# Kernel tuning notes

Measured on AMD Instinct MI355X. Metric: run time of the kernel, lower is better.

The kernel has to match this reference:

```python
import jax, jax.numpy as jnp
import numpy as np

B = 32        # num graphs
N = 512       # nodes per graph (equal-sized blocks)
HID = 512     # hidden_dim
H = 8         # num_heads
E = 262144    # num edges
ED = 16       # edge feature dim


def setup_inputs() -> dict:
    key = jax.random.key(0)
    ks = jax.random.split(key, 12)
    x = jax.random.normal(ks[0], (B * N, HID), jnp.float32)
    # contiguous, sorted graph assignment (equal-sized graphs)
    batch = jnp.repeat(jnp.arange(B, dtype=jnp.int64), N)
    # within-graph random edges
    g = jax.random.randint(ks[1], (E,), 0, B)
    src = g * N + jax.random.randint(ks[2], (E,), 0, N)
    dst = g * N + jax.random.randint(ks[3], (E,), 0, N)
    edge_index = jnp.stack([src, dst]).astype(jnp.int64)
    edge_attr = jax.random.normal(ks[4], (E, ED), jnp.float32)
    s = 1.0 / np.sqrt(HID).astype(np.float32)
    Wq = jax.random.normal(ks[5], (HID, HID), jnp.float32) * s
    Wk = jax.random.normal(ks[6], (HID, HID), jnp.float32) * s
    Wv = jax.random.normal(ks[7], (HID, HID), jnp.float32) * s
    Wo = jax.random.normal(ks[8], (HID, HID), jnp.float32) * s
    We = jax.random.normal(ks[9], (ED, H), jnp.float32) * (1.0 / np.sqrt(ED).astype(np.float32))
    bq = jnp.zeros((HID,), jnp.float32)
    bk = jnp.zeros((HID,), jnp.float32)
    bv = jnp.zeros((HID,), jnp.float32)
    bo = jnp.zeros((HID,), jnp.float32)
    be = jnp.zeros((H,), jnp.float32)
    return dict(x=x, batch=batch, edge_index=edge_index, edge_attr=edge_attr,
                Wq=Wq, bq=bq, Wk=Wk, bk=bk, Wv=Wv, bv=bv, Wo=Wo, bo=bo,
                We=We, be=be, num_graphs=B)


def reference(x, batch, edge_index, edge_attr, Wq, bq, Wk, bk, Wv, bv, Wo, bo, We, be, num_graphs):
    n_total, hid = x.shape
    n = n_total // num_graphs           # nodes per graph (equal blocks)
    hd = hid // H                       # head_dim
    scale = 1.0 / jnp.sqrt(jnp.asarray(hd, x.dtype))
    q = (x @ Wq + bq).reshape(num_graphs, n, H, hd)
    k = (x @ Wk + bk).reshape(num_graphs, n, H, hd)
    v = (x @ Wv + bv).reshape(num_graphs, n, H, hd)
    # per-graph dense scores: [B, n(query), m(key), H]
    attn = jnp.einsum('bnhd,bmhd->bnmh', q, k) * scale
    # edge-bias scatter-add (edges are intra-graph; local coords via div/mod)
    eb = edge_attr @ We + be                      # [E, H]
    b_idx = edge_index[0] // n
    loc_src = edge_index[0] % n
    loc_dst = edge_index[1] % n
    attn = attn.at[b_idx, loc_src, loc_dst].add(eb)
    # softmax over key axis (torch dim=1 of 'nmh' == axis 2 here)
    attn = jax.nn.softmax(attn, axis=2)
    out = jnp.einsum('bnmh,bmhd->bnhd', attn, v).reshape(n_total, hid)
    return out @ Wo + bo
```

## Files before the change

### kernel.cpp

```cpp
#include <hip/hip_runtime.h>
#include <stdint.h>

typedef unsigned short u16;
typedef __bf16 bf16x8 __attribute__((ext_vector_type(8)));
typedef short  short8 __attribute__((ext_vector_type(8)));
typedef float  f32x4  __attribute__((ext_vector_type(4)));
typedef float  float4v __attribute__((ext_vector_type(4)));
typedef uint32_t u32x2 __attribute__((ext_vector_type(2)));

#define NG    32
#define NPG   512
#define HIDD  512
#define NH    8
#define HD    64
#define NE    262144
#define NNODE (NG*NPG)

__device__ __forceinline__ float fexp2(float x) { return __builtin_amdgcn_exp2f(x); }

__device__ __forceinline__ u16 f2bf(float f) {
  union { float f; uint32_t u; } x; x.f = f;
  uint32_t r = x.u + 0x7FFFu + ((x.u >> 16) & 1u);
  return (u16)(r >> 16);
}
__device__ __forceinline__ float bf2f(u16 b) {
  union { uint32_t u; float f; } x; x.u = ((uint32_t)b) << 16;
  return x.f;
}
__device__ __forceinline__ uint32_t pkbf(float a, float b) {
  __bf16 x = (__bf16)a, y = (__bf16)b;
  return (uint32_t)__builtin_bit_cast(u16, x) | ((uint32_t)__builtin_bit_cast(u16, y) << 16);
}
__device__ __forceinline__ bf16x8 ldfrag(const u16* p) {
  short8 t = *(const short8*)p;
  return __builtin_bit_cast(bf16x8, t);
}
__device__ __forceinline__ f32x4 mfma16(bf16x8 a, bf16x8 b, f32x4 c) {
  return __builtin_amdgcn_mfma_f32_16x16x32_bf16(a, b, c, 0, 0, 0);
}
__device__ __forceinline__ void gl2lds16(const void* g, void* l) {
  __builtin_amdgcn_global_load_lds((const __attribute__((address_space(1))) void*)g,
                                   (__attribute__((address_space(3))) void*)l, 16, 0, 0);
}
__device__ __forceinline__ void st(u16* p, float v)   { *p = f2bf(v); }
__device__ __forceinline__ void st(float* p, float v) { *p = v; }


__global__ void k_prep(const float* __restrict__ x, u16* __restrict__ xb,
                       const float* __restrict__ W0, const float* __restrict__ W1,
                       const float* __restrict__ W2, const float* __restrict__ W3,
                       u16* __restrict__ wt,
                       const int* __restrict__ ei, int* __restrict__ counts) {
  __shared__ float tl[32][33];
  const int bid = blockIdx.x, t = threadIdx.x;
  if (bid < 4096) {
    size_t i = ((size_t)bid * 256 + t) * 8;
    float4v v0 = *(const float4v*)(x + i);
    float4v v1 = *(const float4v*)(x + i + 4);
    short8 r;
    r[0]=(short)f2bf(v0[0]); r[1]=(short)f2bf(v0[1]); r[2]=(short)f2bf(v0[2]); r[3]=(short)f2bf(v0[3]);
    r[4]=(short)f2bf(v1[0]); r[5]=(short)f2bf(v1[1]); r[6]=(short)f2bf(v1[2]); r[7]=(short)f2bf(v1[3]);
    *(short8*)(xb + i) = r;
  } else if (bid < 5120) {
    const int id2 = bid - 4096;
    const int z = id2 >> 8, rem = id2 & 255;
    const int y0 = (rem >> 4) * 32, x0 = (rem & 15) * 32;
    const float* W = z==0 ? W0 : z==1 ? W1 : z==2 ? W2 : W3;
    u16* out = wt + (size_t)z * HIDD * HIDD;
    const int tx = t & 31, ty = t >> 5;
    #pragma unroll
    for (int i = 0; i < 4; ++i) tl[ty + i*8][tx] = W[(size_t)(y0 + ty + i*8) * HIDD + x0 + tx];
    __syncthreads();
    #pragma unroll
    for (int i = 0; i < 4; ++i) out[(size_t)(x0 + ty + i*8) * HIDD + (y0 + tx)] = f2bf(tl[tx][ty + i*8]);
  } else {
    int e = (bid - 5120) * 256 + t;
    int src = ei[e];
    int dl  = ei[NE + e] & (NPG - 1);
    atomicAdd(&counts[src * 8 + (dl >> 6)], 1);
  }
}


__global__ void k_scan_u(const int* __restrict__ counts, int* __restrict__ rowstart,
                         int* __restrict__ rowend, int* __restrict__ gcur) {
  __shared__ int arr[256];
  __shared__ int basesh;
  const int t = threadIdx.x;
  const int i = blockIdx.x * 256 + t;
  const int c = counts[i];
  arr[t] = c;
  __syncthreads();
  for (int off = 1; off < 256; off <<= 1) {
    int v = (t >= off) ? arr[t - off] : 0;
    __syncthreads();
    arr[t] += v;
    __syncthreads();
  }
  const int incl = arr[t];
  if (t == 255) basesh = atomicAdd(gcur, incl);
  __syncthreads();
  const int base = basesh;
  rowstart[i] = base + incl - c;
  rowend[i]   = base + incl;
}

__global__ void k_fill(const int* __restrict__ ei, const float* __restrict__ ea,
                       const float* __restrict__ We, const float* __restrict__ be,
                       const int* __restrict__ rowstart, int* __restrict__ cursor,
                       uint32_t* __restrict__ packed) {
  __shared__ float w[128];
  __shared__ float bb[8];
  int t = threadIdx.x;
  if (t < 128) w[t] = We[t];
  if (t < 8)   bb[t] = be[t];
  __syncthreads();
  int e = blockIdx.x * 256 + t;
  int src = ei[e];
  int dl  = ei[NE + e] & (NPG - 1);
  const float* ap = ea + (size_t)e * 16;
  float a[16];
  #pragma unroll
  for (int i = 0; i < 16; i += 4) {
    float4v v = *(const float4v*)(ap + i);
    a[i]=v[0]; a[i+1]=v[1]; a[i+2]=v[2]; a[i+3]=v[3];
  }
  float acc[8];
  #pragma unroll
  for (int hh = 0; hh < 8; ++hh) acc[hh] = bb[hh];
  #pragma unroll
  for (int d = 0; d < 16; ++d)
    #pragma unroll
    for (int hh = 0; hh < 8; ++hh) acc[hh] += a[d] * w[d*8 + hh];
  int bin = src * 8 + (dl >> 6);
  int pos = atomicAdd(&cursor[bin], 1);
  size_t base = ((size_t)(rowstart[bin] + pos)) * 8;
  #pragma unroll
  for (int hh = 0; hh < 8; ++hh) {
    float m = fexp2(acc[hh] * 1.44269504089f);
    union { _Float16 hf; u16 us; } cv; cv.hf = (_Float16)m;
    packed[base + hh] = (uint32_t)(dl & 63) | ((uint32_t)cv.us << 16);
  }
}


template <typename OT, bool VOUT>
__device__ void gemm_body(u16* smem, const u16* __restrict__ A, const u16* __restrict__ Bt,
                          const float* __restrict__ bias, OT* __restrict__ C,
                          u16* __restrict__ vtg, float oscale) {
  const int tid = threadIdx.x;
  const int w = tid >> 6, l = tid & 63, lr = l & 15, lg = l >> 4;
  const int idl = blockIdx.x + (blockIdx.y << 2);
  const int nid = (idl & 7) * 64 + (idl >> 3);
  const int bn0 = (nid & 3) * 128, bm0 = (nid >> 2) * 128;
  const int wr = w >> 1, wc = w & 1;
  f32x4 acc[4][4];
  #pragma unroll
  for (int i = 0; i < 4; ++i)
    #pragma unroll
    for (int j = 0; j < 4; ++j) acc[i][j] = (f32x4){0.f, 0.f, 0.f, 0.f};

  const int o1 = w * 1024 + l * 16;
  auto stageAB = [&](int kt, int buf) {
    #pragma unroll
    for (int rnd = 0; rnd < 2; ++rnd) {
      const int o = rnd * 4096 + o1;
      const int row = o >> 6, colb = o & 63;
      gl2lds16((const char*)A  + ((size_t)(bm0 + row) * HIDD + kt * 32) * 2 + colb,
               (char*)smem + buf * 8192 + o);
      gl2lds16((const char*)Bt + ((size_t)(bn0 + row) * HIDD + kt * 32) * 2 + colb,
               (char*)smem + 16384 + buf * 8192 + o);
    }
  };

  stageAB(0, 0);
  for (int kt = 0; kt < 16; ++kt) {
    if (kt < 15) {
      stageAB(kt + 1, (kt + 1) & 1);
      asm volatile("s_waitcnt vmcnt(4)" ::: "memory");
    } else {
      asm volatile("s_waitcnt vmcnt(0)" ::: "memory");
    }
    __syncthreads();
    const u16* Ab = smem + (kt & 1) * 4096;
    const u16* Bb = smem + 8192 + (kt & 1) * 4096;
    bf16x8 af[4], bfr[4];
    #pragma unroll
    for (int i = 0; i < 4; ++i) af[i]  = ldfrag(&Ab[(wr*64 + i*16 + lr) * 32 + lg*8]);
    #pragma unroll
    for (int j = 0; j < 4; ++j) bfr[j] = ldfrag(&Bb[(wc*64 + j*16 + lr) * 32 + lg*8]);
    #pragma unroll
    for (int i = 0; i < 4; ++i)
      #pragma unroll
      for (int j = 0; j < 4; ++j)
        acc[i][j] = mfma16(af[i], bfr[j], acc[i][j]);
    __syncthreads();
  }

  if constexpr (VOUT) {
    #pragma unroll
    for (int j = 0; j < 4; ++j) {
      const int d = j * 16 + lr;
      const float bv = bias[bn0 + wc*64 + j*16 + lr];
      #pragma unroll
      for (int i = 0; i < 4; ++i) {
        const int t4 = wc * 2 + wr;
        const int byteo = t4 * 8192 + d * 128 + ((i*32 + lg*8) ^ ((d & 7) << 4));
        uint32_t lo = pkbf(acc[i][j][0] + bv, acc[i][j][1] + bv);
        uint32_t hi = pkbf(acc[i][j][2] + bv, acc[i][j][3] + bv);
        *(u32x2*)((char*)smem + byteo) = (u32x2){lo, hi};
      }
    }
    __syncthreads();
    const int b = bm0 >> 9, kt0 = (bm0 & 511) >> 6, h0 = bn0 >> 6;
    #pragma unroll
    for (int t4 = 0; t4 < 4; ++t4) {
      size_t base = ((size_t)(b * 8 + h0 + (t4 >> 1)) * 8 + kt0 + (t4 & 1)) * 4096;
      #pragma unroll
      for (int rnd = 0; rnd < 2; ++rnd) {
        int idx = rnd * 256 + tid;
        *(short8*)(vtg + base + idx * 8) = *(const short8*)&smem[t4 * 4096 + idx * 8];
      }
    }
  } else {
    #pragma unroll
    for (int j = 0; j < 4; ++j) {
      const int col = bn0 + wc*64 + j*16 + lr;
      const float bv = bias[col];
      #pragma unroll
      for (int i = 0; i < 4; ++i) {
        const int row0 = bm0 + wr*64 + i*16 + lg*4;
        #pragma unroll
        for (int q = 0; q < 4; ++q)
          st(&C[(size_t)(row0 + q) * HIDD + col], (acc[i][j][q] + bv) * oscale);
      }
    }
  }
}

__global__ __launch_bounds__(256, 3) void k_gemm_qkv(
    const u16* __restrict__ A, const u16* __restrict__ Wt,
    const float* __restrict__ b0, const float* __restrict__ b1, const float* __restrict__ b2,
    u16* __restrict__ O0, u16* __restrict__ O1, u16* __restrict__ vtg) {
  __shared__ u16 smem[16384];
  const float c1 = 0.125f * 1.44269504089f;
  int z = blockIdx.z;
  const u16* Bt = Wt + (size_t)z * HIDD * HIDD;
  if (z == 0)      gemm_body<u16, false>(smem, A, Bt, b0, O0, nullptr, c1);
  else if (z == 1) gemm_body<u16, false>(smem, A, Bt, b1, O1, nullptr, 1.0f);
  else             gemm_body<u16, true >(smem, A, Bt, b2, nullptr, vtg, 1.0f);
}

__global__ __launch_bounds__(256, 3) void k_gemm_out(
    const u16* __restrict__ A, const u16* __restrict__ Bt,
    const float* __restrict__ bias, float* __restrict__ C) {
  __shared__ u16 smem[16384];
  gemm_body<float, false>(smem, A, Bt, bias, C, nullptr, 1.0f);
}


__global__ __launch_bounds__(256, 4) void k_attn(
    const u16* __restrict__ qb, const u16* __restrict__ kb, const u16* __restrict__ vtg,
    const uint32_t* __restrict__ packed, const int* __restrict__ rowstart2,
    const int* __restrict__ rowend2, u16* __restrict__ ab) {
  __shared__ u16 kl[4096];
  __shared__ u16 vl[4096];
  __shared__ u16 pl[4][2048];
  const int tid = threadIdx.x, w = tid >> 6, l = tid & 63, lr = l & 15, lg = l >> 4;

  const int id = blockIdx.x;
  const int nid = (id & 7) * 128 + (id >> 3);
  const int q0 = (nid & 3) * 128;
  const int h  = (nid >> 2) & 7;
  const int b  = nid >> 5;
  const int bh = b * 8 + h;
  const int rbase = q0 + w * 32;
  u16* plw = &pl[w][0];
  const int pswz = (lr & 7) << 4;

  bf16x8 qf[2][2];
  #pragma unroll
  for (int g = 0; g < 2; ++g) {
    const u16* qp = qb + (size_t)(b * NPG + rbase + g * 16 + lr) * HIDD + h * HD + lg * 8;
    qf[g][0] = ldfrag(qp);
    qf[g][1] = ldfrag(qp + 32);
  }

  auto stageK = [&](int kt) {
    #pragma unroll
    for (int rnd = 0; rnd < 2; ++rnd) {
      int o = rnd * 4096 + w * 1024 + l * 16;
      int key = o >> 7, db = o & 127;
      int col = db ^ ((key & 7) << 4);
      gl2lds16((const char*)kb + ((size_t)(b * NPG + kt * 64 + key) * HIDD + h * HD) * 2 + col,
               (char*)kl + o);
    }
  };
  auto stageV = [&](int kt) {
    #pragma unroll
    for (int rnd = 0; rnd < 2; ++rnd) {
      int o = rnd * 4096 + w * 1024 + l * 16;
      gl2lds16((const char*)vtg + ((size_t)(bh * 8 + kt)) * 8192 + o,
               (char*)vl + o);
    }
  };

  float rs[2] = {0.f, 0.f};
  f32x4 oacc[2][4];
  #pragma unroll
  for (int g = 0; g < 2; ++g)
    #pragma unroll
    for (int dt = 0; dt < 4; ++dt) oacc[g][dt] = (f32x4){0.f, 0.f, 0.f, 0.f};

  stageK(0); stageV(0);

  const int ge = lg & 1, ecls = lg >> 1;
  const int egrow = b * NPG + rbase + ge * 16 + lr;
  int eA = rowstart2[egrow * 8];
  int eE = rowend2[egrow * 8];

  for (int kt = 0; kt < 8; ++kt) {
    asm volatile("s_waitcnt vmcnt(0)" ::: "memory");
    __syncthreads();

    int sN = (kt < 7) ? rowstart2[egrow * 8 + kt + 1] : 0;
    int eN = (kt < 7) ? rowend2[egrow * 8 + kt + 1] : 0;
    int s0c = (eA < eE) ? eA : 0;
    uint32_t u0 = packed[(size_t)s0c * 8 + h];

    f32x4 s4[2][4];
    __builtin_amdgcn_s_setprio(1);
    #pragma unroll
    for (int sub = 0; sub < 4; ++sub) {
      int key = sub * 16 + lr;
      bf16x8 kf0, kf1;
      {
        int db0 = ((lg * 8) * 2) ^ ((key & 7) << 4);
        int db1 = ((32 + lg * 8) * 2) ^ ((key & 7) << 4);
        kf0 = ldfrag(&kl[(key * 128 + db0) >> 1]);
        kf1 = ldfrag(&kl[(key * 128 + db1) >> 1]);
      }
      #pragma unroll
      for (int g = 0; g < 2; ++g) {
        s4[g][sub] = mfma16(kf0, qf[g][0], (f32x4){0.f, 0.f, 0.f, 0.f});
        s4[g][sub] = mfma16(kf1, qf[g][1], s4[g][sub]);
      }
    }
    __builtin_amdgcn_s_setprio(0);

    #pragma unroll
    for (int g = 0; g < 2; ++g) {
      const int prow = g * 16 + lr;
      #pragma unroll
      for (int sub = 0; sub < 4; ++sub) {
        float p0 = fexp2(s4[g][sub][0]);
        float p1 = fexp2(s4[g][sub][1]);
        float p2 = fexp2(s4[g][sub][2]);
        float p3 = fexp2(s4[g][sub][3]);
        rs[g] += (p0 + p1) + (p2 + p3);
        uint32_t lo = pkbf(p0, p1);
        uint32_t hi = pkbf(p2, p3);
        *(u32x2*)((char*)plw + prow * 128 + ((sub * 32 + lg * 8) ^ pswz)) = (u32x2){lo, hi};
      }
    }
    asm volatile("s_waitcnt lgkmcnt(0)" ::: "memory");
    __builtin_amdgcn_sched_barrier(0);

    {
      float delta = 0.f;
      const int re = ge * 16 + lr;
      uint32_t u = u0;
      for (int s = eA; s < eE; ++s) {
        uint32_t ucur = u;
        if (s + 1 < eE) u = packed[(size_t)(s + 1) * 8 + h];
        int dl = (int)(ucur & 63u);
        if ((dl & 1) == ecls) {
          union { u16 us; _Float16 hf; } cv; cv.us = (u16)(ucur >> 16);
          float mult = (float)cv.hf;
          int idx = (re * 128 + ((dl * 2) ^ pswz)) >> 1;
          float old = bf2f(plw[idx]);
          plw[idx] = f2bf(old * mult);
          delta += old * (mult - 1.0f);
        }
      }
      rs[0] += (ge == 0) ? delta : 0.f;
      rs[1] += (ge == 1) ? delta : 0.f;
    }
    asm volatile("s_waitcnt lgkmcnt(0)" ::: "memory");
    __builtin_amdgcn_sched_barrier(0);

    __builtin_amdgcn_s_setprio(1);
    #pragma unroll
    for (int ks = 0; ks < 2; ++ks) {
      bf16x8 pa0 = ldfrag(&plw[(lr * 128 + ((ks * 64 + lg * 16) ^ pswz)) >> 1]);
      bf16x8 pa1 = ldfrag(&plw[((16 + lr) * 128 + ((ks * 64 + lg * 16) ^ pswz)) >> 1]);
      #pragma unroll
      for (int dt = 0; dt < 4; ++dt) {
        int d = dt * 16 + lr;
        bf16x8 vf = ldfrag(&vl[(d * 128 + ((ks * 64 + lg * 16) ^ ((d & 7) << 4))) >> 1]);
        oacc[0][dt] = mfma16(vf, pa0, oacc[0][dt]);
        oacc[1][dt] = mfma16(vf, pa1, oacc[1][dt]);
      }
    }
    __builtin_amdgcn_s_setprio(0);

    __syncthreads();
    if (kt < 7) { stageK(kt + 1); stageV(kt + 1); }
    eA = sN; eE = eN;
  }

  #pragma unroll
  for (int g = 0; g < 2; ++g) {
    float tot = rs[g] + __shfl_xor(rs[g], 16, 64);
    tot += __shfl_xor(tot, 32, 64);
    float inv = 1.0f / tot;
    const size_t grow = (size_t)(b * NPG + rbase + g * 16 + lr);
    #pragma unroll
    for (int dt = 0; dt < 4; ++dt) {
      uint32_t lo = pkbf(oacc[g][dt][0] * inv, oacc[g][dt][1] * inv);
      uint32_t hi = pkbf(oacc[g][dt][2] * inv, oacc[g][dt][3] * inv);
      *(u32x2*)(ab + grow * HIDD + h * HD + dt * 16 + lg * 4) = (u32x2){lo, hi};
    }
  }
}


extern "C" void kernel_launch(void* const* d_in, const int* in_sizes, int n_in,
                              void* d_out, int out_size, void* d_ws, size_t ws_size,
                              hipStream_t stream) {
  const float* x  = (const float*)d_in[0];
  const int*   ei = (const int*)d_in[2];
  const float* ea = (const float*)d_in[3];
  const float* Wq = (const float*)d_in[4];  const float* bq = (const float*)d_in[5];
  const float* Wk = (const float*)d_in[6];  const float* bk = (const float*)d_in[7];
  const float* Wv = (const float*)d_in[8];  const float* bv = (const float*)d_in[9];
  const float* Wo = (const float*)d_in[10]; const float* bo = (const float*)d_in[11];
  const float* We = (const float*)d_in[12]; const float* be = (const float*)d_in[13];

  char* ws = (char*)d_ws;
  const size_t MB = 1 << 20;
  u16*  xb  = (u16*)(ws);
  u16*  wt  = (u16*)(ws + 16*MB);
  u16*  qbp = (u16*)(ws + 18*MB);
  u16*  kbp = (u16*)(ws + 34*MB);
  u16*  vtg = (u16*)(ws + 50*MB);
  uint32_t* packed = (uint32_t*)(ws + 66*MB);
  int*  rowstart2 = (int*)(ws + 74*MB);
  int*  rowend2   = (int*)(ws + 74*MB + 640*1024);
  int*  counts2  = (int*)(ws + 50*MB);
  int*  cursor2  = (int*)(ws + 50*MB + 512*1024);
  int*  gcur     = (int*)(ws + 51*MB);
  u16*  ab = xb;

  (void)hipMemsetAsync(counts2, 0, 1024 * 1024 + 64, stream);

  k_prep<<<dim3(6144), 256, 0, stream>>>(x, xb, Wq, Wk, Wv, Wo, wt, ei, counts2);
  k_scan_u<<<dim3(512), 256, 0, stream>>>(counts2, rowstart2, rowend2, gcur);
  k_fill<<<dim3(NE / 256), 256, 0, stream>>>(ei, ea, We, be, rowstart2, cursor2, packed);

  k_gemm_qkv<<<dim3(HIDD / 128, NNODE / 128, 3), 256, 0, stream>>>(
      xb, wt, bq, bk, bv, qbp, kbp, vtg);

  k_attn<<<dim3(1024), 256, 0, stream>>>(qbp, kbp, vtg, packed, rowstart2, rowend2, ab);

  k_gemm_out<<<dim3(HIDD / 128, NNODE / 128, 1), 256, 0, stream>>>(
      ab, wt + (size_t)3 * HIDD * HIDD, bo, (float*)d_out);
}
```

Before: 159.3 us.

## Fuse edge-fill into QKV GEMM launch and pack row bounds into one word

Merges the edge-bias fill kernel and the QKV projection GEMM into a single launch, with the first 1024 blocks doing edge packing and the rest the GEMM tiles. This removes one kernel launch and lets the two independent jobs overlap. The fill now atomically increments rowstart directly, so the separate cursor array and its memset go away. Row end and count are packed into one uint32, so the attention kernel does one load per bin instead of two. The packing limits per-bin counts to 127 and relies on rowstart being mutated in place.

```diff
diff --git a/kernel.cpp b/kernel.cpp
--- a/kernel.cpp
+++ b/kernel.cpp
@@ -83,7 +83,7 @@
 
 
 __global__ void k_scan_u(const int* __restrict__ counts, int* __restrict__ rowstart,
-                         int* __restrict__ rowend, int* __restrict__ gcur) {
+                         uint32_t* __restrict__ rowse, int* __restrict__ gcur) {
   __shared__ int arr[256];
   __shared__ int basesh;
   const int t = threadIdx.x;
@@ -100,57 +100,18 @@
   const int incl = arr[t];
   if (t == 255) basesh = atomicAdd(gcur, incl);
   __syncthreads();
-  const int base = basesh;
-  rowstart[i] = base + incl - c;
-  rowend[i]   = base + incl;
-}
-
-__global__ void k_fill(const int* __restrict__ ei, const float* __restrict__ ea,
-                       const float* __restrict__ We, const float* __restrict__ be,
-                       const int* __restrict__ rowstart, int* __restrict__ cursor,
-                       uint32_t* __restrict__ packed) {
-  __shared__ float w[128];
-  __shared__ float bb[8];
-  int t = threadIdx.x;
-  if (t < 128) w[t] = We[t];
-  if (t < 8)   bb[t] = be[t];
-  __syncthreads();
-  int e = blockIdx.x * 256 + t;
-  int src = ei[e];
-  int dl  = ei[NE + e] & (NPG - 1);
-  const float* ap = ea + (size_t)e * 16;
-  float a[16];
-  #pragma unroll
-  for (int i = 0; i < 16; i += 4) {
-    float4v v = *(const float4v*)(ap + i);
-    a[i]=v[0]; a[i+1]=v[1]; a[i+2]=v[2]; a[i+3]=v[3];
-  }
-  float acc[8];
-  #pragma unroll
-  for (int hh = 0; hh < 8; ++hh) acc[hh] = bb[hh];
-  #pragma unroll
-  for (int d = 0; d < 16; ++d)
-    #pragma unroll
-    for (int hh = 0; hh < 8; ++hh) acc[hh] += a[d] * w[d*8 + hh];
-  int bin = src * 8 + (dl >> 6);
-  int pos = atomicAdd(&cursor[bin], 1);
-  size_t base = ((size_t)(rowstart[bin] + pos)) * 8;
-  #pragma unroll
-  for (int hh = 0; hh < 8; ++hh) {
-    float m = fexp2(acc[hh] * 1.44269504089f);
-    union { _Float16 hf; u16 us; } cv; cv.hf = (_Float16)m;
-    packed[base + hh] = (uint32_t)(dl & 63) | ((uint32_t)cv.us << 16);
-  }
+  const int end = basesh + incl;
+  rowstart[i] = end - c;
+  rowse[i] = ((uint32_t)end << 7) | (uint32_t)(c & 127);
 }
 
 
 template <typename OT, bool VOUT>
-__device__ void gemm_body(u16* smem, const u16* __restrict__ A, const u16* __restrict__ Bt,
-                          const float* __restrict__ bias, OT* __restrict__ C,
-                          u16* __restrict__ vtg, float oscale) {
+__device__ void gemm_body(u16* smem, int idl, const u16* __restrict__ A,
+                          const u16* __restrict__ Bt, const float* __restrict__ bias,
+                          OT* __restrict__ C, u16* __restrict__ vtg, float oscale) {
   const int tid = threadIdx.x;
   const int w = tid >> 6, l = tid & 63, lr = l & 15, lg = l >> 4;
-  const int idl = blockIdx.x + (blockIdx.y << 2);
   const int nid = (idl & 7) * 64 + (idl >> 3);
   const int bn0 = (nid & 3) * 128, bm0 = (nid >> 2) * 128;
   const int wr = w >> 1, wc = w & 1;
@@ -238,31 +199,72 @@
   }
 }
 
-__global__ __launch_bounds__(256, 3) void k_gemm_qkv(
+
+__global__ __launch_bounds__(256, 3) void k_mid(
+    const int* __restrict__ ei, const float* __restrict__ ea,
+    const float* __restrict__ We, const float* __restrict__ be,
+    int* __restrict__ rowcur, uint32_t* __restrict__ packed,
     const u16* __restrict__ A, const u16* __restrict__ Wt,
     const float* __restrict__ b0, const float* __restrict__ b1, const float* __restrict__ b2,
     u16* __restrict__ O0, u16* __restrict__ O1, u16* __restrict__ vtg) {
   __shared__ u16 smem[16384];
-  const float c1 = 0.125f * 1.44269504089f;
-  int z = blockIdx.z;
-  const u16* Bt = Wt + (size_t)z * HIDD * HIDD;
-  if (z == 0)      gemm_body<u16, false>(smem, A, Bt, b0, O0, nullptr, c1);
-  else if (z == 1) gemm_body<u16, false>(smem, A, Bt, b1, O1, nullptr, 1.0f);
-  else             gemm_body<u16, true >(smem, A, Bt, b2, nullptr, vtg, 1.0f);
+  const int bid = blockIdx.x, t = threadIdx.x;
+  if (bid < 1024) {
+    float* w  = (float*)smem;
+    float* bb = (float*)smem + 128;
+    if (t < 128) w[t] = We[t];
+    if (t < 8)   bb[t] = be[t];
+    __syncthreads();
+    int e = bid * 256 + t;
+    int src = ei[e];
+    int dl  = ei[NE + e] & (NPG - 1);
+    const float* ap = ea + (size_t)e * 16;
+    float a[16];
+    #pragma unroll
+    for (int i = 0; i < 16; i += 4) {
+      float4v v = *(const float4v*)(ap + i);
+      a[i]=v[0]; a[i+1]=v[1]; a[i+2]=v[2]; a[i+3]=v[3];
+    }
+    float acc[8];
+    #pragma unroll
+    for (int hh = 0; hh < 8; ++hh) acc[hh] = bb[hh];
+    #pragma unroll
+    for (int d = 0; d < 16; ++d)
+      #pragma unroll
+      for (int hh = 0; hh < 8; ++hh) acc[hh] += a[d] * w[d*8 + hh];
+    int bin = src * 8 + (dl >> 6);
+    int slot = atomicAdd(&rowcur[bin], 1);
+    size_t base = (size_t)slot * 8;
+    #pragma unroll
+    for (int hh = 0; hh < 8; ++hh) {
+      float m = fexp2(acc[hh] * 1.44269504089f);
+      union { _Float16 hf; u16 us; } cv; cv.hf = (_Float16)m;
+      packed[base + hh] = (uint32_t)(dl & 63) | ((uint32_t)cv.us << 16);
+    }
+  } else {
+    const int idx = bid - 1024;
+    const int z = idx >> 9, idl = idx & 511;
+    const float c1 = 0.125f * 1.44269504089f;
+    const u16* Bt = Wt + (size_t)z * HIDD * HIDD;
+    if (z == 0)      gemm_body<u16, false>(smem, idl, A, Bt, b0, O0, nullptr, c1);
+    else if (z == 1) gemm_body<u16, false>(smem, idl, A, Bt, b1, O1, nullptr, 1.0f);
+    else             gemm_body<u16, true >(smem, idl, A, Bt, b2, nullptr, vtg, 1.0f);
+  }
 }
 
 __global__ __launch_bounds__(256, 3) void k_gemm_out(
     const u16* __restrict__ A, const u16* __restrict__ Bt,
     const float* __restrict__ bias, float* __restrict__ C) {
   __shared__ u16 smem[16384];
-  gemm_body<float, false>(smem, A, Bt, bias, C, nullptr, 1.0f);
+  gemm_body<float, false>(smem, blockIdx.x + (blockIdx.y << 2), A, Bt, bias, C,
+                          nullptr, 1.0f);
 }
 
 
 __global__ __launch_bounds__(256, 4) void k_attn(
     const u16* __restrict__ qb, const u16* __restrict__ kb, const u16* __restrict__ vtg,
-    const uint32_t* __restrict__ packed, const int* __restrict__ rowstart2,
-    const int* __restrict__ rowend2, u16* __restrict__ ab) {
+    const uint32_t* __restrict__ packed, const uint32_t* __restrict__ rowse,
+    u16* __restrict__ ab) {
   __shared__ u16 kl[4096];
   __shared__ u16 vl[4096];
   __shared__ u16 pl[4][2048];
@@ -316,15 +318,14 @@
 
   const int ge = lg & 1, ecls = lg >> 1;
   const int egrow = b * NPG + rbase + ge * 16 + lr;
-  int eA = rowstart2[egrow * 8];
-  int eE = rowend2[egrow * 8];
+  uint32_t ub = rowse[egrow * 8];
+  int eE = (int)(ub >> 7), eA = eE - (int)(ub & 127u);
 
   for (int kt = 0; kt < 8; ++kt) {
     asm volatile("s_waitcnt vmcnt(0)" ::: "memory");
     __syncthreads();
 
-    int sN = (kt < 7) ? rowstart2[egrow * 8 + kt + 1] : 0;
-    int eN = (kt < 7) ? rowend2[egrow * 8 + kt + 1] : 0;
+    uint32_t uN = (kt < 7) ? rowse[egrow * 8 + kt + 1] : 0;
     int s0c = (eA < eE) ? eA : 0;
     uint32_t u0 = packed[(size_t)s0c * 8 + h];
 
@@ -406,7 +407,7 @@
 
     __syncthreads();
     if (kt < 7) { stageK(kt + 1); stageV(kt + 1); }
-    eA = sN; eE = eN;
+    eE = (int)(uN >> 7); eA = eE - (int)(uN & 127u);
   }
 
   #pragma unroll
@@ -445,23 +446,21 @@
   u16*  kbp = (u16*)(ws + 34*MB);
   u16*  vtg = (u16*)(ws + 50*MB);
   uint32_t* packed = (uint32_t*)(ws + 66*MB);
-  int*  rowstart2 = (int*)(ws + 74*MB);
-  int*  rowend2   = (int*)(ws + 74*MB + 640*1024);
-  int*  counts2  = (int*)(ws + 50*MB);
-  int*  cursor2  = (int*)(ws + 50*MB + 512*1024);
-  int*  gcur     = (int*)(ws + 51*MB);
+  int*      rowstart2 = (int*)(ws + 74*MB);
+  uint32_t* rowse     = (uint32_t*)(ws + 74*MB + 640*1024);
+  int*  counts2 = (int*)(ws + 50*MB);
+  int*  gcur    = (int*)(ws + 50*MB + 512*1024);
   u16*  ab = xb;
 
-  (void)hipMemsetAsync(counts2, 0, 1024 * 1024 + 64, stream);
+  (void)hipMemsetAsync(counts2, 0, 512 * 1024 + 64, stream);
 
   k_prep<<<dim3(6144), 256, 0, stream>>>(x, xb, Wq, Wk, Wv, Wo, wt, ei, counts2);
-  k_scan_u<<<dim3(512), 256, 0, stream>>>(counts2, rowstart2, rowend2, gcur);
-  k_fill<<<dim3(NE / 256), 256, 0, stream>>>(ei, ea, We, be, rowstart2, cursor2, packed);
-
-  k_gemm_qkv<<<dim3(HIDD / 128, NNODE / 128, 3), 256, 0, stream>>>(
-      xb, wt, bq, bk, bv, qbp, kbp, vtg);
-
-  k_attn<<<dim3(1024), 256, 0, stream>>>(qbp, kbp, vtg, packed, rowstart2, rowend2, ab);
+  k_scan_u<<<dim3(512), 256, 0, stream>>>(counts2, rowstart2, rowse, gcur);
+
+  k_mid<<<dim3(2560), 256, 0, stream>>>(ei, ea, We, be, rowstart2, packed,
+                                        xb, wt, bq, bk, bv, qbp, kbp, vtg);
+
+  k_attn<<<dim3(1024), 256, 0, stream>>>(qbp, kbp, vtg, packed, rowse, ab);
 
   k_gemm_out<<<dim3(HIDD / 128, NNODE / 128, 1), 256, 0, stream>>>(
       ab, wt + (size_t)3 * HIDD * HIDD, bo, (float*)d_out);
```

Measured after the change: 152.6 us. 1.04x faster.
